# Kernel tuning notes

Measured on AMD Instinct MI355X. Metric: run time of the kernel, lower is better.

The kernel has to match this reference:

```python
import jax, jax.numpy as jnp
import numpy as np

D_MODEL, D_KV, N_HEADS = 1024, 64, 16
NUM_BUCKETS, MAX_DIST = 32, 128
B, S = 2, 2048


def _relative_position_bucket(relative_position, num_buckets=NUM_BUCKETS, max_distance=MAX_DIST):
    # bidirectional=True branch of the TF code
    nb = num_buckets // 2
    n = -relative_position
    ret = (n < 0).astype(jnp.int32) * nb
    n = jnp.abs(n)
    max_exact = nb // 2
    is_small = n < max_exact
    val_if_large = max_exact + (
        jnp.log(n.astype(jnp.float32) / max_exact)
        / np.log(max_distance / max_exact)
        * (nb - max_exact)
    ).astype(jnp.int32)
    val_if_large = jnp.minimum(val_if_large, nb - 1)
    return ret + jnp.where(is_small, n, val_if_large)


def compute_bias(rel_emb, qlen, klen):
    ctx = jnp.arange(qlen)[:, None]
    mem = jnp.arange(klen)[None, :]
    rp_bucket = _relative_position_bucket(mem - ctx)  # [q, k]
    values = rel_emb[rp_bucket]                       # [q, k, h]
    return jnp.transpose(values, (2, 0, 1))[None]     # [1, h, q, k]


def setup_inputs() -> dict:
    key = jax.random.key(0)
    ks = jax.random.split(key, 6)
    sc = 1.0 / np.sqrt(D_MODEL)
    return {
        "inputs": jax.random.normal(ks[0], (B, S, D_MODEL), jnp.float32),
        "Wq": jax.random.normal(ks[1], (D_MODEL, N_HEADS * D_KV), jnp.float32) * sc,
        "Wk": jax.random.normal(ks[2], (D_MODEL, N_HEADS * D_KV), jnp.float32) * sc,
        "Wv": jax.random.normal(ks[3], (D_MODEL, N_HEADS * D_KV), jnp.float32) * sc,
        "Wo": jax.random.normal(ks[4], (N_HEADS * D_KV, D_MODEL), jnp.float32) * sc,
        "rel_emb": jax.random.normal(ks[5], (NUM_BUCKETS, N_HEADS), jnp.float32),
    }


def reference(inputs, Wq, Wk, Wv, Wo, rel_emb):
    bs, qlen, _ = inputs.shape

    def split_heads(x):
        return jnp.transpose(x.reshape(bs, -1, N_HEADS, D_KV), (0, 2, 1, 3))

    q = split_heads(inputs @ Wq)  # [b, h, s, d]
    k = split_heads(inputs @ Wk)
    v = split_heads(inputs @ Wv)

    position_bias = compute_bias(rel_emb, qlen, qlen)      # [1, h, q, k]
    scores = jnp.einsum('bnqd,bnkd->bnqk', q, k) + position_bias  # NOTE: no 1/sqrt(d) scaling (T5 style)
    attn = jax.nn.softmax(scores, axis=-1)
    hidden = jnp.einsum('bnqk,bnkd->bnqd', attn, v)
    hidden = jnp.transpose(hidden, (0, 2, 1, 3)).reshape(bs, qlen, N_HEADS * D_KV)
    return hidden @ Wo
```

## Files before the change

### kernel.cpp

```cpp
#include <hip/hip_runtime.h>


typedef __attribute__((ext_vector_type(8))) short s16x8;
typedef __attribute__((ext_vector_type(4))) float f32x4;
typedef __attribute__((ext_vector_type(16))) float f32x16;
typedef __attribute__((ext_vector_type(2))) unsigned int u32x2;

#if __has_builtin(__builtin_amdgcn_exp2f)
#define EXP2(x) __builtin_amdgcn_exp2f(x)
#else
#define EXP2(x) exp2f(x)
#endif

__device__ __forceinline__ unsigned short f2bf(float f) {
  unsigned int u = __float_as_uint(f);
  u = (u + 0x7fffu + ((u >> 16) & 1u)) >> 16;
  return (unsigned short)u;
}

__device__ __forceinline__ unsigned cvtpk(float lo, float hi) {
  unsigned r;
  asm("v_cvt_pk_bf16_f32 %0, %1, %2" : "=v"(r) : "v"(lo), "v"(hi));
  return r;
}

#define GLD16(g, l)                                              \
  __builtin_amdgcn_global_load_lds(                              \
      (const __attribute__((address_space(1))) void*)(g),        \
      (__attribute__((address_space(3))) void*)(l), 16, 0, 0)

__global__ __launch_bounds__(256) void cvt_lin(const float* __restrict__ in,
                                               unsigned short* __restrict__ out,
                                               int n4) {
  int i = blockIdx.x * 256 + threadIdx.x;
  int stride = gridDim.x * 256;
  for (; i < n4; i += stride) {
    float4 v = ((const float4*)in)[i];
    ushort4 o;
    o.x = f2bf(v.x); o.y = f2bf(v.y); o.z = f2bf(v.z); o.w = f2bf(v.w);
    ((ushort4*)out)[i] = o;
  }
}

__global__ __launch_bounds__(256) void cvt_prep(const float* __restrict__ W0,
                                                const float* __restrict__ W1,
                                                const float* __restrict__ W2,
                                                const float* __restrict__ W3,
                                                const float* __restrict__ rel,
                                                unsigned short* __restrict__ Dqkv,
                                                unsigned short* __restrict__ Do_,
                                                float* __restrict__ tab) {
  const int z = blockIdx.z;
  if (z == 4) {
    int idx = (blockIdx.y * 32 + blockIdx.x) * 256 + threadIdx.x;
    if (idx >= 16 * 4096) return;
    int h = idx >> 12, di = idx & 4095;
    int delta = di - 2047;
    int n = -delta;
    int ret = (n < 0) ? 16 : 0;
    n = n < 0 ? -n : n;
    int bucket;
    if (n < 8) {
      bucket = ret + n;
    } else {
      float lf = (float)log((double)n * 0.125);
      float f = lf / 2.772588722239781f * 8.0f;
      int v = 8 + (int)f;
      bucket = ret + (v < 15 ? v : 15);
    }
    tab[idx] = rel[bucket * 16 + h] * 1.4426950408889634f;
    return;
  }
  const float* W = (z == 0) ? W0 : (z == 1) ? W1 : (z == 2) ? W2 : W3;
  unsigned short* WT = (z < 3) ? (Dqkv + (size_t)z * 1024 * 1024) : Do_;
  __shared__ float t[32][33];
  int n0 = blockIdx.x * 32, k0 = blockIdx.y * 32;
  int tx = threadIdx.x & 31, ty = threadIdx.x >> 5;
#pragma unroll
  for (int i = 0; i < 32; i += 8)
    t[ty + i][tx] = W[(size_t)(k0 + ty + i) * 1024 + n0 + tx];
  __syncthreads();
#pragma unroll
  for (int i = 0; i < 32; i += 8)
    WT[(size_t)(n0 + ty + i) * 1024 + k0 + tx] = f2bf(t[tx][ty + i]);
}

__global__ __launch_bounds__(256, 2) void gemm_qkv(
    const unsigned short* __restrict__ A, const unsigned short* __restrict__ BT,
    unsigned short* __restrict__ O0, unsigned short* __restrict__ O1,
    unsigned short* __restrict__ O2) {
  __shared__ __align__(16) unsigned short aT[128 * 64];
  __shared__ __align__(16) unsigned short bT[128 * 64];
  const int tid = threadIdx.x;
  const int lane = tid & 63, w = tid >> 6;
  const int l15 = lane & 15, l4 = lane >> 4;
  const int m0 = blockIdx.y * 128, n0 = blockIdx.x * 128;
  const int wr = w >> 1, wc = w & 1;

  const f32x4 fzero = {0.f, 0.f, 0.f, 0.f};
  f32x4 acc[4][4];
#pragma unroll
  for (int i = 0; i < 4; ++i)
#pragma unroll
    for (int j = 0; j < 4; ++j) acc[i][j] = fzero;

  for (int k0 = 0; k0 < 1024; k0 += 64) {
#pragma unroll
    for (int p = 0; p < 4; ++p) {
      int slot = (p * 4 + w) * 64 + lane;
      int row = slot >> 3, s = slot & 7;
      int ks = (s ^ (row & 7)) << 3;
      GLD16(A + (size_t)(m0 + row) * 1024 + k0 + ks, (char*)aT + (p * 4 + w) * 1024);
      GLD16(BT + (size_t)(n0 + row) * 1024 + k0 + ks, (char*)bT + (p * 4 + w) * 1024);
    }
    __syncthreads();
#pragma unroll
    for (int kk = 0; kk < 2; ++kk) {
      int slotk = kk * 4 + l4;
      s16x8 af[4], bfr[4];
#pragma unroll
      for (int mi = 0; mi < 4; ++mi) {
        int row = wr * 64 + mi * 16 + l15;
        af[mi] = *(const s16x8*)(aT + row * 64 + ((slotk ^ (row & 7)) << 3));
      }
#pragma unroll
      for (int nj = 0; nj < 4; ++nj) {
        int row = wc * 64 + nj * 16 + l15;
        bfr[nj] = *(const s16x8*)(bT + row * 64 + ((slotk ^ (row & 7)) << 3));
      }
      __builtin_amdgcn_s_setprio(1);
#pragma unroll
      for (int mi = 0; mi < 4; ++mi)
#pragma unroll
        for (int nj = 0; nj < 4; ++nj)
          acc[mi][nj] = __builtin_amdgcn_mfma_f32_16x16x32_bf16(af[mi], bfr[nj], acc[mi][nj], 0, 0, 0);
      __builtin_amdgcn_s_setprio(0);
    }
    __syncthreads();
  }

#pragma unroll
  for (int mi = 0; mi < 4; ++mi)
#pragma unroll
    for (int nj = 0; nj < 4; ++nj)
#pragma unroll
      for (int r = 0; r < 4; ++r) {
        int row = m0 + wr * 64 + mi * 16 + l4 * 4 + r;
        int col = n0 + wc * 64 + nj * 16 + l15;
        int which = col >> 10;
        int cc = col & 1023;
        int b = row >> 11, s2 = row & 2047, hh = cc >> 6, d = cc & 63;
        if (which == 0)
          O0[((size_t)((b * 16 + hh) * 2048 + s2)) * 64 + d] =
              f2bf(acc[mi][nj][r] * 1.4426950408889634f);
        else if (which == 1)
          O1[((size_t)((b * 16 + hh) * 2048 + s2)) * 64 + d] = f2bf(acc[mi][nj][r]);
        else
          O2[((size_t)((b * 16 + hh) * 64 + d)) * 2048 + s2] = f2bf(acc[mi][nj][r]);
      }
}

__global__ __launch_bounds__(256, 2) void gemm_op(
    const unsigned short* __restrict__ A, const unsigned short* __restrict__ BT,
    float* __restrict__ O) {
  __shared__ __align__(16) unsigned short aT[128 * 64];
  __shared__ __align__(16) unsigned short bT[64 * 64];
  const int tid = threadIdx.x;
  const int lane = tid & 63, w = tid >> 6;
  const int l15 = lane & 15, l4 = lane >> 4;
  const int m0 = blockIdx.y * 128, n0 = blockIdx.x * 64;
  const int wr = w >> 1, wc = w & 1;

  const f32x4 fzero = {0.f, 0.f, 0.f, 0.f};
  f32x4 acc[4][2];
#pragma unroll
  for (int i = 0; i < 4; ++i)
#pragma unroll
    for (int j = 0; j < 2; ++j) acc[i][j] = fzero;

  for (int k0 = 0; k0 < 1024; k0 += 64) {
#pragma unroll
    for (int p = 0; p < 4; ++p) {
      int slot = (p * 4 + w) * 64 + lane;
      int row = slot >> 3, s = slot & 7;
      int ks = (s ^ (row & 7)) << 3;
      GLD16(A + (size_t)(m0 + row) * 1024 + k0 + ks, (char*)aT + (p * 4 + w) * 1024);
    }
#pragma unroll
    for (int p = 0; p < 2; ++p) {
      int slot = (p * 4 + w) * 64 + lane;
      int row = slot >> 3, s = slot & 7;
      int ks = (s ^ (row & 7)) << 3;
      GLD16(BT + (size_t)(n0 + row) * 1024 + k0 + ks, (char*)bT + (p * 4 + w) * 1024);
    }
    __syncthreads();
#pragma unroll
    for (int kk = 0; kk < 2; ++kk) {
      int slotk = kk * 4 + l4;
      s16x8 af[4], bfr[2];
#pragma unroll
      for (int mi = 0; mi < 4; ++mi) {
        int row = wr * 64 + mi * 16 + l15;
        af[mi] = *(const s16x8*)(aT + row * 64 + ((slotk ^ (row & 7)) << 3));
      }
#pragma unroll
      for (int nj = 0; nj < 2; ++nj) {
        int row = wc * 32 + nj * 16 + l15;
        bfr[nj] = *(const s16x8*)(bT + row * 64 + ((slotk ^ (row & 7)) << 3));
      }
      __builtin_amdgcn_s_setprio(1);
#pragma unroll
      for (int mi = 0; mi < 4; ++mi)
#pragma unroll
        for (int nj = 0; nj < 2; ++nj)
          acc[mi][nj] = __builtin_amdgcn_mfma_f32_16x16x32_bf16(af[mi], bfr[nj], acc[mi][nj], 0, 0, 0);
      __builtin_amdgcn_s_setprio(0);
    }
    __syncthreads();
  }

#pragma unroll
  for (int mi = 0; mi < 4; ++mi)
#pragma unroll
    for (int nj = 0; nj < 2; ++nj)
#pragma unroll
      for (int r = 0; r < 4; ++r) {
        int row = m0 + wr * 64 + mi * 16 + l4 * 4 + r;
        int col = n0 + wc * 32 + nj * 16 + l15;
        O[(size_t)row * 1024 + col] = acc[mi][nj][r];
      }
}

__global__ __launch_bounds__(512, 2) void attn_k(
    const unsigned short* __restrict__ Q,
    const unsigned short* __restrict__ K,
    const unsigned short* __restrict__ VT,
    const float* __restrict__ btab,
    unsigned short* __restrict__ H) {
  __shared__ __align__(16) char smem[65536];
  const int tid = threadIdx.x;
  const int lane = tid & 63, w = tid >> 6;
  const int l31 = lane & 31, l5 = lane >> 5;
  const int half = w >> 2;
  const int L = blockIdx.x;
  const int qtile = (L >> 3) & 15, bh = (L & 7) * 4 + (L >> 7);
  const int q0 = qtile * 128 + (w & 3) * 32;
  const int h = bh & 15, b = bh >> 4;
  const unsigned short* Qp = Q + (size_t)bh * 2048 * 64;
  const unsigned short* Kp = K + (size_t)bh * 2048 * 64;
  const unsigned short* Vp = VT + (size_t)bh * 64 * 2048;
  const float* btq = btab + h * 4096 + 2047 - (q0 + l31) + 4 * l5 + half * 1024;

#define STAGE(buf, kvv)                                                              \
  {                                                                                  \
    int row_ = tid >> 3, s_ = tid & 7;                                               \
    int ks_ = (s_ ^ (row_ & 7)) << 3;                                                \
    GLD16(Kp + (size_t)((kvv) + row_) * 64 + ks_, smem + (buf) * 8192 + tid * 16);   \
    GLD16(Kp + (size_t)(1024 + (kvv) + row_) * 64 + ks_,                             \
          smem + 32768 + (buf) * 8192 + tid * 16);                                   \
    GLD16(Vp + (size_t)row_ * 2048 + (kvv) + ks_,                                    \
          smem + 16384 + (buf) * 8192 + tid * 16);                                   \
    GLD16(Vp + (size_t)row_ * 2048 + 1024 + (kvv) + ks_,                             \
          smem + 16384 + 32768 + (buf) * 8192 + tid * 16);                           \
  }

  s16x8 qf[4];
#pragma unroll
  for (int ks = 0; ks < 4; ++ks)
    qf[ks] = *(const s16x8*)(Qp + (size_t)(q0 + l31) * 64 + ks * 16 + l5 * 8);

  f32x16 oacc[2];
#pragma unroll
  for (int r = 0; r < 16; ++r) { oacc[0][r] = 0.f; oacc[1][r] = 0.f; }
  float s4[4] = {0.f, 0.f, 0.f, 0.f};

  STAGE(0, 0);
  __syncthreads();
  int cur = 0;
  const char* kbase = smem + half * 32768;
  const char* vbase = smem + half * 32768 + 16384;

#define BODY(KVV)                                                                    \
  {                                                                                  \
    const int kvv = (KVV);                                                           \
    if (kvv + 64 < 1024) STAGE(cur ^ 1, kvv + 64);                                   \
                               \
    f32x16 st[2];                                                                    \
    _Pragma("unroll") for (int t = 0; t < 2; ++t)                                    \
      _Pragma("unroll") for (int r = 0; r < 16; ++r)                                 \
        st[t][r] = btq[kvv + t * 32 + (r & 3) + 8 * (r >> 2)];                       \
    const char* kl = kbase + cur * 8192;                                             \
    __builtin_amdgcn_s_setprio(1);                                                   \
    _Pragma("unroll") for (int ks = 0; ks < 4; ++ks) {                               \
      int sl = ks * 2 + l5;                                                          \
      int sw = (sl ^ (l31 & 7)) << 4;                                                \
      s16x8 ka0 = *(const s16x8*)(kl + l31 * 128 + sw);                              \
      s16x8 ka1 = *(const s16x8*)(kl + (32 + l31) * 128 + sw);                       \
      st[0] = __builtin_amdgcn_mfma_f32_32x32x16_bf16(ka0, qf[ks], st[0], 0, 0, 0);  \
      st[1] = __builtin_amdgcn_mfma_f32_32x32x16_bf16(ka1, qf[ks], st[1], 0, 0, 0);  \
    }                                                                                \
    __builtin_amdgcn_s_setprio(0);                                                   \
    _Pragma("unroll") for (int t = 0; t < 2; ++t)                                    \
      _Pragma("unroll") for (int r = 0; r < 16; ++r) {                               \
        float p_ = EXP2(st[t][r]);                                                   \
        st[t][r] = p_;                                                               \
        s4[r & 3] += p_;                                                             \
      }                                                                              \
    s16x8 pb[4];                                                                     \
    _Pragma("unroll") for (int t = 0; t < 2; ++t)                                    \
      _Pragma("unroll") for (int hh = 0; hh < 2; ++hh) {                             \
        unsigned cA = cvtpk(st[t][hh * 8 + 0], st[t][hh * 8 + 1]);                   \
        unsigned cB = cvtpk(st[t][hh * 8 + 2], st[t][hh * 8 + 3]);                   \
        unsigned cC = cvtpk(st[t][hh * 8 + 4], st[t][hh * 8 + 5]);                   \
        unsigned cD = cvtpk(st[t][hh * 8 + 6], st[t][hh * 8 + 7]);                   \
        u32x2 s1 = __builtin_amdgcn_permlane32_swap(cA, cC, false, false);           \
        u32x2 s2 = __builtin_amdgcn_permlane32_swap(cB, cD, false, false);           \
        union { unsigned u[4]; s16x8 v; } pu;                                        \
        pu.u[0] = s1.x; pu.u[1] = s2.x; pu.u[2] = s1.y; pu.u[3] = s2.y;              \
        pb[t * 2 + hh] = pu.v;                                                       \
      }                                                                              \
    const char* vl = vbase + cur * 8192;                                             \
    __builtin_amdgcn_s_setprio(1);                                                   \
    _Pragma("unroll") for (int ks2 = 0; ks2 < 4; ++ks2) {                            \
      int sl = ks2 * 2 + l5;                                                         \
      int sw = (sl ^ (l31 & 7)) << 4;                                                \
      s16x8 va0 = *(const s16x8*)(vl + l31 * 128 + sw);                              \
      s16x8 va1 = *(const s16x8*)(vl + (32 + l31) * 128 + sw);                       \
      oacc[0] = __builtin_amdgcn_mfma_f32_32x32x16_bf16(va0, pb[ks2], oacc[0], 0, 0, 0); \
      oacc[1] = __builtin_amdgcn_mfma_f32_32x32x16_bf16(va1, pb[ks2], oacc[1], 0, 0, 0); \
    }                                                                                \
    __builtin_amdgcn_s_setprio(0);                                                   \
    __syncthreads();                                                                 \
    cur ^= 1;                                                                        \
  }

  for (int s = 0; s < 16; ++s) BODY(s * 64);
#undef BODY
#undef STAGE

  float sum = (s4[0] + s4[1]) + (s4[2] + s4[3]);
  u32x2 rs = __builtin_amdgcn_permlane32_swap(__float_as_uint(sum), __float_as_uint(sum), false, false);
  float lsum = __uint_as_float(rs.x) + __uint_as_float(rs.y);

  float* comb = (float*)smem;
  if (w >= 4) {
    float* p = comb + ((w - 4) * 64 + lane) * 34;
#pragma unroll
    for (int r = 0; r < 16; ++r) { p[r] = oacc[0][r]; p[16 + r] = oacc[1][r]; }
    p[32] = lsum;
  }
  __syncthreads();
  if (w < 4) {
    const float* p = comb + (w * 64 + lane) * 34;
#pragma unroll
    for (int r = 0; r < 16; ++r) { oacc[0][r] += p[r]; oacc[1][r] += p[16 + r]; }
    float inv = 1.0f / (lsum + p[32]);
    size_t hb = (((size_t)(b * 2048 + q0 + l31)) * 1024 + h * 64 + 4 * l5) * 2;
#pragma unroll
    for (int nd = 0; nd < 2; ++nd)
#pragma unroll
      for (int g = 0; g < 4; ++g) {
        unsigned w0 = cvtpk(oacc[nd][g * 4 + 0] * inv, oacc[nd][g * 4 + 1] * inv);
        unsigned w1 = cvtpk(oacc[nd][g * 4 + 2] * inv, oacc[nd][g * 4 + 3] * inv);
        unsigned long long pk8 = (unsigned long long)w0 | ((unsigned long long)w1 << 32);
        *(unsigned long long*)((char*)H + hb + (nd * 32 + 8 * g) * 2) = pk8;
      }
  }
}

extern "C" void kernel_launch(void* const* d_in, const int* in_sizes, int n_in,
                              void* d_out, int out_size, void* d_ws, size_t ws_size,
                              hipStream_t stream) {
  const float* X   = (const float*)d_in[0];
  const float* Wq  = (const float*)d_in[1];
  const float* Wk  = (const float*)d_in[2];
  const float* Wv  = (const float*)d_in[3];
  const float* Wo  = (const float*)d_in[4];
  const float* rel = (const float*)d_in[5];

  char* ws = (char*)d_ws;
  unsigned short* Xb     = (unsigned short*)(ws);
  unsigned short* Hid    = Xb;
  unsigned short* WqkvT  = (unsigned short*)(ws + (8u << 20));
  unsigned short* WoT    = (unsigned short*)(ws + (14u << 20));
  unsigned short* Qb     = (unsigned short*)(ws + (16u << 20));
  unsigned short* Kb     = (unsigned short*)(ws + (24u << 20));
  unsigned short* VTb    = (unsigned short*)(ws + (32u << 20));
  float* btab            = (float*)(ws + (40u << 20));

  cvt_lin<<<1024, 256, 0, stream>>>(X, Xb, (2 * 2048 * 1024) / 4);
  cvt_prep<<<dim3(32, 32, 5), 256, 0, stream>>>(Wq, Wk, Wv, Wo, rel, WqkvT, WoT, btab);

  gemm_qkv<<<dim3(24, 32), 256, 0, stream>>>(Xb, WqkvT, Qb, Kb, VTb);

  attn_k<<<512, 512, 0, stream>>>(Qb, Kb, VTb, btab, Hid);

  gemm_op<<<dim3(16, 32), 256, 0, stream>>>(Hid, WoT, (float*)d_out);
}
```

Measured before the change: 118.3 us.

## Software-pipeline attention loop: compute next QK scores before current softmax/PV

Restructures the attention main loop so the QK^T MFMAs for tile i+1 are issued before the exp/convert and PV MFMAs of tile i. It also prefetches K/V two tiles ahead, with double-buffered K and triple-buffered V in a larger 80 KB LDS region. The aim is to overlap MFMA work with the transcendental/conversion work and hide global-load latency. It also raises launch_bounds minimum blocks from 2 to 4, which tightens the register budget and risks spills, while the larger LDS footprint may cap real occupancy.

New measurement: 197.0 us. 1.66x slower.

```diff
diff --git a/kernel.cpp b/kernel.cpp
--- a/kernel.cpp
+++ b/kernel.cpp
@@ -231,13 +231,13 @@
       }
 }
 
-__global__ __launch_bounds__(512, 2) void attn_k(
+__global__ __launch_bounds__(512, 4) void attn_k(
     const unsigned short* __restrict__ Q,
     const unsigned short* __restrict__ K,
     const unsigned short* __restrict__ VT,
     const float* __restrict__ btab,
     unsigned short* __restrict__ H) {
-  __shared__ __align__(16) char smem[65536];
+  __shared__ __align__(16) char smem[81920];
   const int tid = threadIdx.x;
   const int lane = tid & 63, w = tid >> 6;
   const int l31 = lane & 31, l5 = lane >> 5;
@@ -251,17 +251,18 @@
   const unsigned short* Vp = VT + (size_t)bh * 64 * 2048;
   const float* btq = btab + h * 4096 + 2047 - (q0 + l31) + 4 * l5 + half * 1024;
 
-#define STAGE(buf, kvv)                                                              \
+#define KBUF(st_, b_) (smem + (st_) * 40960 + (b_) * 8192)
+#define VBUF(st_, b_) (smem + (st_) * 40960 + 16384 + (b_) * 8192)
+
+#define STAGEKV(T)                                                                   \
   {                                                                                  \
+    const int kvv_ = (T) * 64;                                                       \
     int row_ = tid >> 3, s_ = tid & 7;                                               \
     int ks_ = (s_ ^ (row_ & 7)) << 3;                                                \
-    GLD16(Kp + (size_t)((kvv) + row_) * 64 + ks_, smem + (buf) * 8192 + tid * 16);   \
-    GLD16(Kp + (size_t)(1024 + (kvv) + row_) * 64 + ks_,                             \
-          smem + 32768 + (buf) * 8192 + tid * 16);                                   \
-    GLD16(Vp + (size_t)row_ * 2048 + (kvv) + ks_,                                    \
-          smem + 16384 + (buf) * 8192 + tid * 16);                                   \
-    GLD16(Vp + (size_t)row_ * 2048 + 1024 + (kvv) + ks_,                             \
-          smem + 16384 + 32768 + (buf) * 8192 + tid * 16);                           \
+    GLD16(Kp + (size_t)(kvv_ + row_) * 64 + ks_, KBUF(0, (T) & 1) + tid * 16);       \
+    GLD16(Kp + (size_t)(1024 + kvv_ + row_) * 64 + ks_, KBUF(1, (T) & 1) + tid * 16);\
+    GLD16(Vp + (size_t)row_ * 2048 + kvv_ + ks_, VBUF(0, (T) % 3) + tid * 16);       \
+    GLD16(Vp + (size_t)row_ * 2048 + 1024 + kvv_ + ks_, VBUF(1, (T) % 3) + tid * 16);\
   }
 
   s16x8 qf[4];
@@ -274,52 +275,51 @@
   for (int r = 0; r < 16; ++r) { oacc[0][r] = 0.f; oacc[1][r] = 0.f; }
   float s4[4] = {0.f, 0.f, 0.f, 0.f};
 
-  STAGE(0, 0);
-  __syncthreads();
-  int cur = 0;
-  const char* kbase = smem + half * 32768;
-  const char* vbase = smem + half * 32768 + 16384;
-
-#define BODY(KVV)                                                                    \
+  f32x16 stA[2], stB[2];
+
+#define QK(T, ST)                                                                    \
   {                                                                                  \
-    const int kvv = (KVV);                                                           \
-    if (kvv + 64 < 1024) STAGE(cur ^ 1, kvv + 64);                                   \
-                               \
-    f32x16 st[2];                                                                    \
     _Pragma("unroll") for (int t = 0; t < 2; ++t)                                    \
       _Pragma("unroll") for (int r = 0; r < 16; ++r)                                 \
-        st[t][r] = btq[kvv + t * 32 + (r & 3) + 8 * (r >> 2)];                       \
-    const char* kl = kbase + cur * 8192;                                             \
+        ST[t][r] = btq[(T) * 64 + t * 32 + (r & 3) + 8 * (r >> 2)];                  \
+    const char* kl = KBUF(half, (T) & 1);                                            \
     __builtin_amdgcn_s_setprio(1);                                                   \
     _Pragma("unroll") for (int ks = 0; ks < 4; ++ks) {                               \
       int sl = ks * 2 + l5;                                                          \
       int sw = (sl ^ (l31 & 7)) << 4;                                                \
       s16x8 ka0 = *(const s16x8*)(kl + l31 * 128 + sw);                              \
       s16x8 ka1 = *(const s16x8*)(kl + (32 + l31) * 128 + sw);                       \
-      st[0] = __builtin_amdgcn_mfma_f32_32x32x16_bf16(ka0, qf[ks], st[0], 0, 0, 0);  \
-      st[1] = __builtin_amdgcn_mfma_f32_32x32x16_bf16(ka1, qf[ks], st[1], 0, 0, 0);  \
+      ST[0] = __builtin_amdgcn_mfma_f32_32x32x16_bf16(ka0, qf[ks], ST[0], 0, 0, 0);  \
+      ST[1] = __builtin_amdgcn_mfma_f32_32x32x16_bf16(ka1, qf[ks], ST[1], 0, 0, 0);  \
     }                                                                                \
     __builtin_amdgcn_s_setprio(0);                                                   \
+  }
+
+#define BODY(I, SC, SN)                                                              \
+  {                                                                                  \
+    if ((I) + 2 < 16) STAGEKV((I) + 2);                                              \
+    if ((I) + 1 < 16) QK((I) + 1, SN);                                               \
+                    \
     _Pragma("unroll") for (int t = 0; t < 2; ++t)                                    \
       _Pragma("unroll") for (int r = 0; r < 16; ++r) {                               \
-        float p_ = EXP2(st[t][r]);                                                   \
-        st[t][r] = p_;                                                               \
+        float p_ = EXP2(SC[t][r]);                                                   \
+        SC[t][r] = p_;                                                               \
         s4[r & 3] += p_;                                                             \
       }                                                                              \
     s16x8 pb[4];                                                                     \
     _Pragma("unroll") for (int t = 0; t < 2; ++t)                                    \
       _Pragma("unroll") for (int hh = 0; hh < 2; ++hh) {                             \
-        unsigned cA = cvtpk(st[t][hh * 8 + 0], st[t][hh * 8 + 1]);                   \
-        unsigned cB = cvtpk(st[t][hh * 8 + 2], st[t][hh * 8 + 3]);                   \
-        unsigned cC = cvtpk(st[t][hh * 8 + 4], st[t][hh * 8 + 5]);                   \
-        unsigned cD = cvtpk(st[t][hh * 8 + 6], st[t][hh * 8 + 7]);                   \
+        unsigned cA = cvtpk(SC[t][hh * 8 + 0], SC[t][hh * 8 + 1]);                   \
+        unsigned cB = cvtpk(SC[t][hh * 8 + 2], SC[t][hh * 8 + 3]);                   \
+        unsigned cC = cvtpk(SC[t][hh * 8 + 4], SC[t][hh * 8 + 5]);                   \
+        unsigned cD = cvtpk(SC[t][hh * 8 + 6], SC[t][hh * 8 + 7]);                   \
         u32x2 s1 = __builtin_amdgcn_permlane32_swap(cA, cC, false, false);           \
         u32x2 s2 = __builtin_amdgcn_permlane32_swap(cB, cD, false, false);           \
         union { unsigned u[4]; s16x8 v; } pu;                                        \
         pu.u[0] = s1.x; pu.u[1] = s2.x; pu.u[2] = s1.y; pu.u[3] = s2.y;              \
         pb[t * 2 + hh] = pu.v;                                                       \
       }                                                                              \
-    const char* vl = vbase + cur * 8192;                                             \
+    const char* vl = VBUF(half, (I) % 3);                                            \
     __builtin_amdgcn_s_setprio(1);                                                   \
     _Pragma("unroll") for (int ks2 = 0; ks2 < 4; ++ks2) {                            \
       int sl = ks2 * 2 + l5;                                                         \
@@ -331,12 +331,23 @@
     }                                                                                \
     __builtin_amdgcn_s_setprio(0);                                                   \
     __syncthreads();                                                                 \
-    cur ^= 1;                                                                        \
-  }
-
-  for (int s = 0; s < 16; ++s) BODY(s * 64);
+  }
+
+  STAGEKV(0);
+  STAGEKV(1);
+  __syncthreads();
+  QK(0, stA);
+  __syncthreads();
+
+  for (int s = 0; s < 16; s += 2) {
+    BODY(s, stA, stB);
+    BODY(s + 1, stB, stA);
+  }
 #undef BODY
-#undef STAGE
+#undef QK
+#undef STAGEKV
+#undef KBUF
+#undef VBUF
 
   float sum = (s4[0] + s4[1]) + (s4[2] + s4[3]);
   u32x2 rs = __builtin_amdgcn_permlane32_swap(__float_as_uint(sum), __float_as_uint(sum), false, false);
```
